# Performance work log

Hardware: AMD Instinct MI355X
Metric: run time of the kernel (lower is better)

Reference implementation:

```python
import jax, jax.numpy as jnp
import numpy as np


def setup_inputs() -> dict:
    key = jax.random.key(0)
    k1, k2, k3 = jax.random.split(key, 3)
    B, C, T = 8, 256, 4096
    H, K = 512, 4
    x = jax.random.normal(k1, (B, C, T), dtype=jnp.float32)
    W = jax.random.normal(k2, (H, C * K), dtype=jnp.float32) * 0.02
    b = jax.random.normal(k3, (H,), dtype=jnp.float32) * 0.02
    return {"x": x, "W": W, "b": b}


def reference(x, W, b):
    # Causal conv1d equivalent of the per-step Linear loop (stride=1).
    # Original flattens window as view(B, C*K): channel-major -> W[h, c*K + k].
    B, C, T = x.shape
    H = W.shape[0]
    K = W.shape[1] // C
    kernel = W.reshape(H, C, K)  # OIH layout
    out = jax.lax.conv_general_dilated(
        x, kernel,
        window_strides=(1,),
        padding=[(K - 1, 0)],  # left-pad only => causal
        dimension_numbers=("NCH", "OIH", "NCH"),
    )
    return out + b[None, :, None]  # (B, H, T)
```

## Files before the change

kernel.cpp:

```cpp
#include <hip/hip_runtime.h>
#include <hip/hip_bf16.h>


#define Bb 8
#define Cc 256
#define Tt 4096
#define Hh 512
#define Kk 4

typedef __attribute__((ext_vector_type(8))) short bf16x8;
typedef __attribute__((ext_vector_type(4))) float f32x4;

#define WS_XT_OFF   0
#define WS_WT_OFF   16777216
#define WS_ZERO_OFF 17825792
#define WS_NEEDED   17826816ULL

__device__ __forceinline__ void gload16(const void* g, void* l) {
    __builtin_amdgcn_global_load_lds(
        (const __attribute__((address_space(1))) void*)g,
        (__attribute__((address_space(3))) void*)l, 16, 0, 0);
}

__global__ __launch_bounds__(256) void prep_kernel(const float* __restrict__ x,
                                                   const float* __restrict__ W,
                                                   __hip_bfloat16* __restrict__ xT,
                                                   __hip_bfloat16* __restrict__ Wt,
                                                   float* __restrict__ zeros) {
    __shared__ __hip_bfloat16 tile[64][72];
    const int bid = blockIdx.x;
    if (bid < 2048) {
        const int t0 = (bid & 63) * 64, c0 = ((bid >> 6) & 3) * 64, b = bid >> 8;
        const int lt = threadIdx.x & 63, lw = threadIdx.x >> 6;
#pragma unroll
        for (int i = 0; i < 16; ++i) {
            int cc = lw + i * 4;
            tile[cc][lt] = __float2bfloat16(x[((size_t)(b * Cc + c0 + cc)) * Tt + t0 + lt]);
        }
        __syncthreads();
#pragma unroll
        for (int i = 0; i < 2; ++i) {
            int tt = (threadIdx.x >> 3) + i * 32;
            int c8 = threadIdx.x & 7;
            short tmp[8];
#pragma unroll
            for (int j = 0; j < 8; ++j) {
                __hip_bfloat16 v = tile[c8 * 8 + j][tt];
                tmp[j] = *reinterpret_cast<short*>(&v);
            }
            *reinterpret_cast<bf16x8*>(&xT[((size_t)(b * Tt + t0 + tt)) * Cc + c0 + c8 * 8]) =
                *reinterpret_cast<bf16x8*>(tmp);
        }
    } else {
        int n = (bid - 2048) * 256 + threadIdx.x;
        int c = n & 255;
        int h = (n >> 8) & 511;
        int k = n >> 17;
        Wt[n] = __float2bfloat16(W[h * (Cc * Kk) + c * Kk + k]);
        if (bid == 2048) zeros[threadIdx.x] = 0.f;
    }
}

#define A_BUF   16384
#define B_BUF   12288
#define B_BASE  49152
#define LDS_TOTAL 73728

#define BAR __builtin_amdgcn_s_barrier()
#define LGKM0 do { asm volatile("s_waitcnt lgkmcnt(0)" ::: "memory"); \
                   __builtin_amdgcn_sched_barrier(0); } while (0)

__global__ __launch_bounds__(256, 2) void conv_mfma_kernel(
    const __hip_bfloat16* __restrict__ xT,
    const __hip_bfloat16* __restrict__ Wt,
    const float* __restrict__ bias,
    const float* __restrict__ zeros,
    float* __restrict__ out)
{
    __shared__ __align__(1024) char smem[LDS_TOTAL];
    const int tid = threadIdx.x, lane = tid & 63, wave = tid >> 6;
    const int wr = wave >> 1, wc = wave & 1;
    const int l15 = lane & 15, lg = lane >> 4;

    const int flat = blockIdx.x + 32 * blockIdx.y + 64 * blockIdx.z;
    const int swz  = (flat & 7) * 64 + (flat >> 3);
    const int t0 = (swz & 31) * 128;
    const int h0 = ((swz >> 5) & 1) * 256;
    const int b  = swz >> 6;

    const char* Wt_c = (const char*)Wt;
    const char* xT_c = (const char*)xT;
    const char* zz   = (const char*)zeros;

    const char* abase[4]; int adst_[4];
#pragma unroll
    for (int i = 0; i < 4; ++i) {
        int s = tid + i * 256;
        int row = s >> 2, sl = s & 3;
        int colch = (sl ^ ((row >> 1) & 3)) * 8;
        abase[i] = Wt_c + (((size_t)(h0 + row)) * Cc + colch) * 2;
        adst_[i] = s * 16;
    }
    const char* bbase[3]; int bdst_[3];
#pragma unroll
    for (int i = 0; i < 3; ++i) {
        int s = tid + i * 256;
        int row = s >> 2, sl = s & 3;
        int colch = (sl ^ ((row >> 1) & 3)) * 8;
        int tg = t0 - 3 + row;
        bool valid = (row <= 130) && (tg >= 0);
        bbase[i] = valid ? xT_c + (((size_t)b * Tt + tg) * Cc + colch) * 2
                         : zz + (s & 31) * 16;
        bdst_[i] = s * 16;
    }

    const int aoff0 = (wr * 128 + l15) * 64 + ((lg ^ ((l15 >> 1) & 3)) << 4);
    int btab[4];
#pragma unroll
    for (int k = 0; k < 4; ++k)
        btab[k] = (wc * 64 + l15 + k) * 64 + ((lg ^ (((l15 + k) >> 1) & 3)) << 4);

    char *A0 = smem, *A1 = smem + A_BUF, *A2 = smem + 2 * A_BUF;
    char *B0 = smem + B_BASE, *B1 = smem + B_BASE + B_BUF;

#pragma unroll
    for (int i = 0; i < 4; ++i) gload16(abase[i], A0 + adst_[i]);
#pragma unroll
    for (int i = 0; i < 3; ++i) gload16(bbase[i], B0 + bdst_[i]);
#pragma unroll
    for (int i = 0; i < 4; ++i) gload16(abase[i] + 262144, A1 + adst_[i]);
    asm volatile("s_waitcnt vmcnt(4)" ::: "memory");
    BAR;

    f32x4 acc[8][4] = {};

#pragma unroll 4
    for (int s = 0; s < 32; ++s) {
        const int kap = s & 3;
        const int bo  = (kap == 0) ? btab[0] : (kap == 1) ? btab[1]
                      : (kap == 2) ? btab[2] : btab[3];

        bf16x8 a_[4], b_[4];
#pragma unroll
        for (int fm = 0; fm < 4; ++fm) a_[fm] = *(const bf16x8*)(A0 + aoff0 + fm * 1024);
#pragma unroll
        for (int ft = 0; ft < 4; ++ft) b_[ft] = *(const bf16x8*)(B0 + bo + ft * 1024);
        if (s < 30) {
            const long au = (long)((s + 2) & 3) * 262144 + (long)((s + 2) >> 2) * 64;
#pragma unroll
            for (int i = 0; i < 4; ++i) gload16(abase[i] + au, A2 + adst_[i]);
        }
        BAR; LGKM0;
        __builtin_amdgcn_s_setprio(1);
#pragma unroll
        for (int fm = 0; fm < 4; ++fm)
#pragma unroll
            for (int ft = 0; ft < 4; ++ft)
                acc[fm][ft] = __builtin_amdgcn_mfma_f32_16x16x32_bf16(a_[fm], b_[ft], acc[fm][ft], 0, 0, 0);
        __builtin_amdgcn_s_setprio(0);
        BAR;
#pragma unroll
        for (int fm = 0; fm < 4; ++fm) a_[fm] = *(const bf16x8*)(A0 + aoff0 + (fm + 4) * 1024);
        if (kap == 0 && s < 28) {
            const long bu = (long)((s >> 2) + 1) * 64;
#pragma unroll
            for (int i = 0; i < 3; ++i) gload16(bbase[i] + bu, B1 + bdst_[i]);
        }
        BAR; LGKM0;
        __builtin_amdgcn_s_setprio(1);
#pragma unroll
        for (int fm = 0; fm < 4; ++fm)
#pragma unroll
            for (int ft = 0; ft < 4; ++ft)
                acc[fm + 4][ft] = __builtin_amdgcn_mfma_f32_16x16x32_bf16(a_[fm], b_[ft], acc[fm + 4][ft], 0, 0, 0);
        __builtin_amdgcn_s_setprio(0);
        if (s < 30) {
            if (kap == 0 && s < 28) asm volatile("s_waitcnt vmcnt(7)" ::: "memory");
            else                    asm volatile("s_waitcnt vmcnt(4)" ::: "memory");
        } else if (s == 30)         asm volatile("s_waitcnt vmcnt(0)" ::: "memory");
        BAR;
        char* tp = A0; A0 = A1; A1 = A2; A2 = tp;
        if (kap == 3) { char* up = B0; B0 = B1; B1 = up; }
    }

#pragma unroll
    for (int fm = 0; fm < 8; ++fm) {
        int hb = h0 + wr * 128 + fm * 16 + lg * 4;
        float4 bs = *(const float4*)&bias[hb];
        const float* bsp = (const float*)&bs;
#pragma unroll
        for (int q = 0; q < 4; ++q)
#pragma unroll
            for (int ft = 0; ft < 4; ++ft) {
                int t = t0 + wc * 64 + ft * 16 + l15;
                out[((size_t)(b * Hh + hb + q)) * Tt + t] = acc[fm][ft][q] + bsp[q];
            }
    }
}

#define TT 256
#define HT 8
#define CT 4
__global__ __launch_bounds__(256) void conv1d_f32_kernel(
    const float* __restrict__ x, const float* __restrict__ W,
    const float* __restrict__ bias, float* __restrict__ out)
{
    const int tid = threadIdx.x;
    const int t0 = blockIdx.x * TT;
    const int h0 = blockIdx.y * HT;
    const int b  = blockIdx.z;
    __shared__ float xs[CT][TT + Kk];
    float acc[HT];
#pragma unroll
    for (int h = 0; h < HT; ++h) acc[h] = 0.f;
    const float* xb = x + (size_t)b * Cc * Tt;
    for (int c0 = 0; c0 < Cc; c0 += CT) {
        __syncthreads();
#pragma unroll
        for (int cc = 0; cc < CT; ++cc)
            for (int j = tid; j < TT + Kk - 1; j += 256) {
                int idx = t0 - (Kk - 1) + j;
                xs[cc][j] = (idx >= 0) ? xb[(size_t)(c0 + cc) * Tt + idx] : 0.f;
            }
        __syncthreads();
#pragma unroll
        for (int cc = 0; cc < CT; ++cc) {
            float xv[Kk];
#pragma unroll
            for (int k = 0; k < Kk; ++k) xv[k] = xs[cc][tid + k];
#pragma unroll
            for (int h = 0; h < HT; ++h) {
                const float* wp = W + (size_t)(h0 + h) * (Cc * Kk) + (size_t)(c0 + cc) * Kk;
#pragma unroll
                for (int k = 0; k < Kk; ++k) acc[h] += wp[k] * xv[k];
            }
        }
    }
#pragma unroll
    for (int h = 0; h < HT; ++h)
        out[((size_t)b * Hh + (h0 + h)) * Tt + t0 + tid] = acc[h] + bias[h0 + h];
}

extern "C" void kernel_launch(void* const* d_in, const int* in_sizes, int n_in,
                              void* d_out, int out_size, void* d_ws, size_t ws_size,
                              hipStream_t stream) {
    const float* x    = (const float*)d_in[0];
    const float* W    = (const float*)d_in[1];
    const float* bias = (const float*)d_in[2];
    float* out        = (float*)d_out;

    if (ws_size >= WS_NEEDED) {
        __hip_bfloat16* xT = (__hip_bfloat16*)((char*)d_ws + WS_XT_OFF);
        __hip_bfloat16* Wt = (__hip_bfloat16*)((char*)d_ws + WS_WT_OFF);
        float* zeros       = (float*)((char*)d_ws + WS_ZERO_OFF);

        prep_kernel<<<dim3(4096), dim3(256), 0, stream>>>(x, W, xT, Wt, zeros);
        conv_mfma_kernel<<<dim3(32, 2, 8), dim3(256), 0, stream>>>(xT, Wt, bias, zeros, out);
    } else {
        conv1d_f32_kernel<<<dim3(Tt / TT, Hh / HT, Bb), dim3(256), 0, stream>>>(x, W, bias, out);
    }
}
```

Before: 51.14 us.

## Fuse x transpose and bf16 conversion into the conv MFMA kernel

Removes the separate pass that transposed x into a (B,T,C) bf16 workspace copy. The conv kernel now reads fp32 x directly through registers, converts it to bf16 and writes swizzled tiles into LDS inside its pipeline. Only the small weight-prep kernel stays. This drops a 32MB read and a 16MB write plus a launch. In exchange it uses strided per-thread global loads, extra VGPRs and manual vmcnt accounting inside the main loop.

```diff
diff --git a/kernel.cpp b/kernel.cpp
--- a/kernel.cpp
+++ b/kernel.cpp
@@ -11,10 +11,7 @@
 typedef __attribute__((ext_vector_type(8))) short bf16x8;
 typedef __attribute__((ext_vector_type(4))) float f32x4;
 
-#define WS_XT_OFF   0
-#define WS_WT_OFF   16777216
-#define WS_ZERO_OFF 17825792
-#define WS_NEEDED   17826816ULL
+#define WS_NEEDED 1048576ULL
 
 __device__ __forceinline__ void gload16(const void* g, void* l) {
     __builtin_amdgcn_global_load_lds(
@@ -22,43 +19,13 @@
         (__attribute__((address_space(3))) void*)l, 16, 0, 0);
 }
 
-__global__ __launch_bounds__(256) void prep_kernel(const float* __restrict__ x,
-                                                   const float* __restrict__ W,
-                                                   __hip_bfloat16* __restrict__ xT,
-                                                   __hip_bfloat16* __restrict__ Wt,
-                                                   float* __restrict__ zeros) {
-    __shared__ __hip_bfloat16 tile[64][72];
-    const int bid = blockIdx.x;
-    if (bid < 2048) {
-        const int t0 = (bid & 63) * 64, c0 = ((bid >> 6) & 3) * 64, b = bid >> 8;
-        const int lt = threadIdx.x & 63, lw = threadIdx.x >> 6;
-#pragma unroll
-        for (int i = 0; i < 16; ++i) {
-            int cc = lw + i * 4;
-            tile[cc][lt] = __float2bfloat16(x[((size_t)(b * Cc + c0 + cc)) * Tt + t0 + lt]);
-        }
-        __syncthreads();
-#pragma unroll
-        for (int i = 0; i < 2; ++i) {
-            int tt = (threadIdx.x >> 3) + i * 32;
-            int c8 = threadIdx.x & 7;
-            short tmp[8];
-#pragma unroll
-            for (int j = 0; j < 8; ++j) {
-                __hip_bfloat16 v = tile[c8 * 8 + j][tt];
-                tmp[j] = *reinterpret_cast<short*>(&v);
-            }
-            *reinterpret_cast<bf16x8*>(&xT[((size_t)(b * Tt + t0 + tt)) * Cc + c0 + c8 * 8]) =
-                *reinterpret_cast<bf16x8*>(tmp);
-        }
-    } else {
-        int n = (bid - 2048) * 256 + threadIdx.x;
-        int c = n & 255;
-        int h = (n >> 8) & 511;
-        int k = n >> 17;
-        Wt[n] = __float2bfloat16(W[h * (Cc * Kk) + c * Kk + k]);
-        if (bid == 2048) zeros[threadIdx.x] = 0.f;
-    }
+__global__ __launch_bounds__(256) void wt_prep_kernel(const float* __restrict__ W,
+                                                      __hip_bfloat16* __restrict__ Wt) {
+    int n = blockIdx.x * 256 + threadIdx.x;
+    int c = n & 255;
+    int h = (n >> 8) & 511;
+    int k = n >> 17;
+    Wt[n] = __float2bfloat16(W[h * (Cc * Kk) + c * Kk + k]);
 }
 
 #define A_BUF   16384
@@ -70,11 +37,44 @@
 #define LGKM0 do { asm volatile("s_waitcnt lgkmcnt(0)" ::: "memory"); \
                    __builtin_amdgcn_sched_barrier(0); } while (0)
 
+#define BLOADS(csb, vv, vvt) do {                                               \
+    int tg_ = t0 - 3 + (tid >> 1);                                              \
+    const float* xp_ = x + ((size_t)(b * Cc + (csb) + (tid & 1) * 16)) * Tt     \
+                         + (tg_ >= 0 ? tg_ : 0);                                \
+    _Pragma("unroll") for (int j = 0; j < 16; ++j) vv[j] = xp_[(size_t)j * Tt]; \
+    if (tg_ < 0) { _Pragma("unroll") for (int j = 0; j < 16; ++j) vv[j] = 0.f; }\
+    if (tid < 6) {                                                              \
+        const float* xq_ = x + ((size_t)(b * Cc + (csb) + (tid & 1) * 16)) * Tt \
+                             + (t0 - 3 + 128 + (tid >> 1));                     \
+        _Pragma("unroll") for (int j = 0; j < 16; ++j) vvt[j] = xq_[(size_t)j * Tt]; \
+    }                                                                           \
+} while (0)
+
+#define BSTORE(dstbuf, vv, vvt) do {                                            \
+    int r_ = tid >> 1, sw_ = (r_ >> 1) & 3, sl0_ = (tid & 1) * 2;               \
+    short o_[16];                                                               \
+    _Pragma("unroll") for (int j = 0; j < 16; ++j) {                            \
+        __hip_bfloat16 h_ = __float2bfloat16(vv[j]);                            \
+        o_[j] = *reinterpret_cast<short*>(&h_);                                 \
+    }                                                                           \
+    *(bf16x8*)((dstbuf) + r_ * 64 + (((sl0_    ) ^ sw_) << 4)) = *(bf16x8*)&o_[0]; \
+    *(bf16x8*)((dstbuf) + r_ * 64 + (((sl0_ + 1) ^ sw_) << 4)) = *(bf16x8*)&o_[8]; \
+    if (tid < 6) {                                                              \
+        int r2_ = 128 + (tid >> 1), sw2_ = (r2_ >> 1) & 3;                      \
+        short p_[16];                                                           \
+        _Pragma("unroll") for (int j = 0; j < 16; ++j) {                        \
+            __hip_bfloat16 h_ = __float2bfloat16(vvt[j]);                       \
+            p_[j] = *reinterpret_cast<short*>(&h_);                             \
+        }                                                                       \
+        *(bf16x8*)((dstbuf) + r2_ * 64 + (((sl0_    ) ^ sw2_) << 4)) = *(bf16x8*)&p_[0]; \
+        *(bf16x8*)((dstbuf) + r2_ * 64 + (((sl0_ + 1) ^ sw2_) << 4)) = *(bf16x8*)&p_[8]; \
+    }                                                                           \
+} while (0)
+
 __global__ __launch_bounds__(256, 2) void conv_mfma_kernel(
-    const __hip_bfloat16* __restrict__ xT,
+    const float* __restrict__ x,
     const __hip_bfloat16* __restrict__ Wt,
     const float* __restrict__ bias,
-    const float* __restrict__ zeros,
     float* __restrict__ out)
 {
     __shared__ __align__(1024) char smem[LDS_TOTAL];
@@ -89,8 +89,6 @@
     const int b  = swz >> 6;
 
     const char* Wt_c = (const char*)Wt;
-    const char* xT_c = (const char*)xT;
-    const char* zz   = (const char*)zeros;
 
     const char* abase[4]; int adst_[4];
 #pragma unroll
@@ -101,18 +99,6 @@
         abase[i] = Wt_c + (((size_t)(h0 + row)) * Cc + colch) * 2;
         adst_[i] = s * 16;
     }
-    const char* bbase[3]; int bdst_[3];
-#pragma unroll
-    for (int i = 0; i < 3; ++i) {
-        int s = tid + i * 256;
-        int row = s >> 2, sl = s & 3;
-        int colch = (sl ^ ((row >> 1) & 3)) * 8;
-        int tg = t0 - 3 + row;
-        bool valid = (row <= 130) && (tg >= 0);
-        bbase[i] = valid ? xT_c + (((size_t)b * Tt + tg) * Cc + colch) * 2
-                         : zz + (s & 31) * 16;
-        bdst_[i] = s * 16;
-    }
 
     const int aoff0 = (wr * 128 + l15) * 64 + ((lg ^ ((l15 >> 1) & 3)) << 4);
     int btab[4];
@@ -123,14 +109,19 @@
     char *A0 = smem, *A1 = smem + A_BUF, *A2 = smem + 2 * A_BUF;
     char *B0 = smem + B_BASE, *B1 = smem + B_BASE + B_BUF;
 
-#pragma unroll
-    for (int i = 0; i < 4; ++i) gload16(abase[i], A0 + adst_[i]);
-#pragma unroll
-    for (int i = 0; i < 3; ++i) gload16(bbase[i], B0 + bdst_[i]);
-#pragma unroll
-    for (int i = 0; i < 4; ++i) gload16(abase[i] + 262144, A1 + adst_[i]);
-    asm volatile("s_waitcnt vmcnt(4)" ::: "memory");
-    BAR;
+    {
+        float pv[16], pvt[16];
+        BLOADS(0, pv, pvt);
+#pragma unroll
+        for (int i = 0; i < 4; ++i) gload16(abase[i], A0 + adst_[i]);
+#pragma unroll
+        for (int i = 0; i < 4; ++i) gload16(abase[i] + 262144, A1 + adst_[i]);
+        asm volatile("s_waitcnt vmcnt(8)" ::: "memory");
+        BSTORE(B0, pv, pvt);
+        asm volatile("s_waitcnt vmcnt(4)" ::: "memory");
+        asm volatile("s_waitcnt lgkmcnt(0)" ::: "memory");
+        BAR;
+    }
 
     f32x4 acc[8][4] = {};
 
@@ -139,12 +130,15 @@
         const int kap = s & 3;
         const int bo  = (kap == 0) ? btab[0] : (kap == 1) ? btab[1]
                       : (kap == 2) ? btab[2] : btab[3];
-
-        bf16x8 a_[4], b_[4];
+        const bool doB = (kap == 0) && (s < 28);
+
+        float bv_[16], bvt_[16];
+        bf16x8 a_[4], bfr_[4];
 #pragma unroll
         for (int fm = 0; fm < 4; ++fm) a_[fm] = *(const bf16x8*)(A0 + aoff0 + fm * 1024);
 #pragma unroll
-        for (int ft = 0; ft < 4; ++ft) b_[ft] = *(const bf16x8*)(B0 + bo + ft * 1024);
+        for (int ft = 0; ft < 4; ++ft) bfr_[ft] = *(const bf16x8*)(B0 + bo + ft * 1024);
+        if (doB) BLOADS(((s >> 2) + 1) * 32, bv_, bvt_);
         if (s < 30) {
             const long au = (long)((s + 2) & 3) * 262144 + (long)((s + 2) >> 2) * 64;
 #pragma unroll
@@ -156,15 +150,14 @@
         for (int fm = 0; fm < 4; ++fm)
 #pragma unroll
             for (int ft = 0; ft < 4; ++ft)
-                acc[fm][ft] = __builtin_amdgcn_mfma_f32_16x16x32_bf16(a_[fm], b_[ft], acc[fm][ft], 0, 0, 0);
+                acc[fm][ft] = __builtin_amdgcn_mfma_f32_16x16x32_bf16(a_[fm], bfr_[ft], acc[fm][ft], 0, 0, 0);
         __builtin_amdgcn_s_setprio(0);
         BAR;
 #pragma unroll
         for (int fm = 0; fm < 4; ++fm) a_[fm] = *(const bf16x8*)(A0 + aoff0 + (fm + 4) * 1024);
-        if (kap == 0 && s < 28) {
-            const long bu = (long)((s >> 2) + 1) * 64;
-#pragma unroll
-            for (int i = 0; i < 3; ++i) gload16(bbase[i] + bu, B1 + bdst_[i]);
+        if (doB) {
+            asm volatile("s_waitcnt vmcnt(4)" ::: "memory");
+            BSTORE(B1, bv_, bvt_);
         }
         BAR; LGKM0;
         __builtin_amdgcn_s_setprio(1);
@@ -172,12 +165,10 @@
         for (int fm = 0; fm < 4; ++fm)
 #pragma unroll
             for (int ft = 0; ft < 4; ++ft)
-                acc[fm + 4][ft] = __builtin_amdgcn_mfma_f32_16x16x32_bf16(a_[fm], b_[ft], acc[fm + 4][ft], 0, 0, 0);
+                acc[fm + 4][ft] = __builtin_amdgcn_mfma_f32_16x16x32_bf16(a_[fm], bfr_[ft], acc[fm + 4][ft], 0, 0, 0);
         __builtin_amdgcn_s_setprio(0);
-        if (s < 30) {
-            if (kap == 0 && s < 28) asm volatile("s_waitcnt vmcnt(7)" ::: "memory");
-            else                    asm volatile("s_waitcnt vmcnt(4)" ::: "memory");
-        } else if (s == 30)         asm volatile("s_waitcnt vmcnt(0)" ::: "memory");
+        if (s < 30)       asm volatile("s_waitcnt vmcnt(4)" ::: "memory");
+        else if (s == 30) asm volatile("s_waitcnt vmcnt(0)" ::: "memory");
         BAR;
         char* tp = A0; A0 = A1; A1 = A2; A2 = tp;
         if (kap == 3) { char* up = B0; B0 = B1; B1 = up; }
@@ -250,12 +241,9 @@
     float* out        = (float*)d_out;
 
     if (ws_size >= WS_NEEDED) {
-        __hip_bfloat16* xT = (__hip_bfloat16*)((char*)d_ws + WS_XT_OFF);
-        __hip_bfloat16* Wt = (__hip_bfloat16*)((char*)d_ws + WS_WT_OFF);
-        float* zeros       = (float*)((char*)d_ws + WS_ZERO_OFF);
-
-        prep_kernel<<<dim3(4096), dim3(256), 0, stream>>>(x, W, xT, Wt, zeros);
-        conv_mfma_kernel<<<dim3(32, 2, 8), dim3(256), 0, stream>>>(xT, Wt, bias, zeros, out);
+        __hip_bfloat16* Wt = (__hip_bfloat16*)d_ws;
+        wt_prep_kernel<<<dim3((Kk * Hh * Cc) / 256), dim3(256), 0, stream>>>(W, Wt);
+        conv_mfma_kernel<<<dim3(32, 2, 8), dim3(256), 0, stream>>>(x, Wt, bias, out);
     } else {
         conv1d_f32_kernel<<<dim3(Tt / TT, Hh / HT, Bb), dim3(256), 0, stream>>>(x, W, bias, out);
     }
```

New measurement: 72.11 us. +41.0%, slower.

## Shrink conv MFMA tile to 128x128 with double-buffered A/B and 3 blocks/CU

Applied to the files above, without the earlier changes.

Halves the per-block H tile from 256 to 128 rows, so there are 1024 blocks instead of 512, and cuts LDS from 72KB to 50KB to allow three blocks per CU. The A pipeline moves from triple to double buffering. Each stage now loads two kernel taps (k pairs), giving 16 iterations instead of 32, with fewer barriers per iteration. The intent is better occupancy and load balance across CUs. The cost is that the x tile is reloaded twice as often, and prefetch depth is shallower, with stricter vmcnt waits.

```diff
diff --git a/kernel.cpp b/kernel.cpp
--- a/kernel.cpp
+++ b/kernel.cpp
@@ -61,16 +61,16 @@
     }
 }
 
-#define A_BUF   16384
-#define B_BUF   12288
-#define B_BASE  49152
-#define LDS_TOTAL 73728
+#define A_BUF    16384
+#define B_BUF    9216
+#define B_BASE   32768
+#define LDS_TOTAL 51200
 
 #define BAR __builtin_amdgcn_s_barrier()
 #define LGKM0 do { asm volatile("s_waitcnt lgkmcnt(0)" ::: "memory"); \
                    __builtin_amdgcn_sched_barrier(0); } while (0)
 
-__global__ __launch_bounds__(256, 2) void conv_mfma_kernel(
+__global__ __launch_bounds__(256, 3) void conv_mfma_kernel(
     const __hip_bfloat16* __restrict__ xT,
     const __hip_bfloat16* __restrict__ Wt,
     const float* __restrict__ bias,
@@ -82,75 +82,81 @@
     const int wr = wave >> 1, wc = wave & 1;
     const int l15 = lane & 15, lg = lane >> 4;
 
-    const int flat = blockIdx.x + 32 * blockIdx.y + 64 * blockIdx.z;
-    const int swz  = (flat & 7) * 64 + (flat >> 3);
-    const int t0 = (swz & 31) * 128;
-    const int h0 = ((swz >> 5) & 1) * 256;
-    const int b  = swz >> 6;
+    const int flat = blockIdx.x + 32 * blockIdx.y + 128 * blockIdx.z;
+    const int nf   = (flat & 7) * 128 + (flat >> 3);
+    const int h0 = (nf & 3) * 128;
+    const int t0 = ((nf >> 2) & 31) * 128;
+    const int b  = nf >> 7;
 
     const char* Wt_c = (const char*)Wt;
     const char* xT_c = (const char*)xT;
     const char* zz   = (const char*)zeros;
 
-    const char* abase[4]; int adst_[4];
+    const char* asrc[4]; int adst_[4];
 #pragma unroll
     for (int i = 0; i < 4; ++i) {
         int s = tid + i * 256;
-        int row = s >> 2, sl = s & 3;
+        int kk = s >> 9, row = (s >> 2) & 127, sl = s & 3;
         int colch = (sl ^ ((row >> 1) & 3)) * 8;
-        abase[i] = Wt_c + (((size_t)(h0 + row)) * Cc + colch) * 2;
+        asrc[i] = Wt_c + (((size_t)(kk * Hh + h0 + row)) * Cc + colch) * 2;
         adst_[i] = s * 16;
     }
-    const char* bbase[3]; int bdst_[3];
+    const char* bsrc[3]; int bdst_[3]; int bstep[3];
 #pragma unroll
     for (int i = 0; i < 3; ++i) {
-        int s = tid + i * 256;
+        int s = (i < 2) ? tid + i * 256 : 512 + lane;
         int row = s >> 2, sl = s & 3;
         int colch = (sl ^ ((row >> 1) & 3)) * 8;
         int tg = t0 - 3 + row;
         bool valid = (row <= 130) && (tg >= 0);
-        bbase[i] = valid ? xT_c + (((size_t)b * Tt + tg) * Cc + colch) * 2
-                         : zz + (s & 31) * 16;
+        bsrc[i]  = valid ? xT_c + (((size_t)b * Tt + tg) * Cc + colch) * 2
+                         : zz + (s & 15) * 16;
+        bstep[i] = valid ? 64 : 0;
         bdst_[i] = s * 16;
     }
 
-    const int aoff0 = (wr * 128 + l15) * 64 + ((lg ^ ((l15 >> 1) & 3)) << 4);
+    const int aoffb = (wr * 64 + l15) * 64 + ((lg ^ ((l15 >> 1) & 3)) << 4);
     int btab[4];
 #pragma unroll
     for (int k = 0; k < 4; ++k)
         btab[k] = (wc * 64 + l15 + k) * 64 + ((lg ^ (((l15 + k) >> 1) & 3)) << 4);
 
-    char *A0 = smem, *A1 = smem + A_BUF, *A2 = smem + 2 * A_BUF;
-    char *B0 = smem + B_BASE, *B1 = smem + B_BASE + B_BUF;
-
-#pragma unroll
-    for (int i = 0; i < 4; ++i) gload16(abase[i], A0 + adst_[i]);
-#pragma unroll
-    for (int i = 0; i < 3; ++i) gload16(bbase[i], B0 + bdst_[i]);
-#pragma unroll
-    for (int i = 0; i < 4; ++i) gload16(abase[i] + 262144, A1 + adst_[i]);
-    asm volatile("s_waitcnt vmcnt(4)" ::: "memory");
+    f32x4 acc[4][4] = {};
+
+#pragma unroll
+    for (int i = 0; i < 4; ++i) gload16(asrc[i], smem + adst_[i]);
+#pragma unroll
+    for (int i = 0; i < 2; ++i) gload16(bsrc[i], smem + B_BASE + bdst_[i]);
+    if (wave == 0) gload16(bsrc[2], smem + B_BASE + bdst_[2]);
+    asm volatile("s_waitcnt vmcnt(0)" ::: "memory");
     BAR;
 
-    f32x4 acc[8][4] = {};
-
-#pragma unroll 4
-    for (int s = 0; s < 32; ++s) {
-        const int kap = s & 3;
-        const int bo  = (kap == 0) ? btab[0] : (kap == 1) ? btab[1]
-                      : (kap == 2) ? btab[2] : btab[3];
+#pragma unroll
+    for (int s = 0; s < 16; ++s) {
+        const int p  = s >> 1;
+        const int kb = 2 * (s & 1);
+        const char* Ab = smem + (s & 1) * A_BUF;
+        const char* Bbf = smem + B_BASE + (p & 1) * B_BUF;
+
+        if (s < 15) {
+            const long aadv = (long)((s + 1) & 1) * 524288 + (long)((s + 1) >> 1) * 64;
+            char* An = smem + ((s + 1) & 1) * A_BUF;
+#pragma unroll
+            for (int i = 0; i < 4; ++i) gload16(asrc[i] + aadv, An + adst_[i]);
+        }
+        if (((s & 1) == 0) && (p < 7)) {
+            char* Bn = smem + B_BASE + ((p + 1) & 1) * B_BUF;
+#pragma unroll
+            for (int i = 0; i < 2; ++i) gload16(bsrc[i] + (p + 1) * bstep[i], Bn + bdst_[i]);
+            if (wave == 0) gload16(bsrc[2] + (p + 1) * bstep[2], Bn + bdst_[2]);
+        }
 
         bf16x8 a_[4], b_[4];
 #pragma unroll
-        for (int fm = 0; fm < 4; ++fm) a_[fm] = *(const bf16x8*)(A0 + aoff0 + fm * 1024);
-#pragma unroll
-        for (int ft = 0; ft < 4; ++ft) b_[ft] = *(const bf16x8*)(B0 + bo + ft * 1024);
-        if (s < 30) {
-            const long au = (long)((s + 2) & 3) * 262144 + (long)((s + 2) >> 2) * 64;
-#pragma unroll
-            for (int i = 0; i < 4; ++i) gload16(abase[i] + au, A2 + adst_[i]);
-        }
-        BAR; LGKM0;
+        for (int fm = 0; fm < 4; ++fm) a_[fm] = *(const bf16x8*)(Ab + aoffb + fm * 1024);
+#pragma unroll
+        for (int ft = 0; ft < 4; ++ft) b_[ft] = *(const bf16x8*)(Bbf + btab[kb] + ft * 1024);
+        LGKM0;
         __builtin_amdgcn_s_setprio(1);
 #pragma unroll
         for (int fm = 0; fm < 4; ++fm)
@@ -158,34 +164,29 @@
             for (int ft = 0; ft < 4; ++ft)
                 acc[fm][ft] = __builtin_amdgcn_mfma_f32_16x16x32_bf16(a_[fm], b_[ft], acc[fm][ft], 0, 0, 0);
         __builtin_amdgcn_s_setprio(0);
-        BAR;
-#pragma unroll
-        for (int fm = 0; fm < 4; ++fm) a_[fm] = *(const bf16x8*)(A0 + aoff0 + (fm + 4) * 1024);
-        if (kap == 0 && s < 28) {
-            const long bu = (long)((s >> 2) + 1) * 64;
-#pragma unroll
-            for (int i = 0; i < 3; ++i) gload16(bbase[i] + bu, B1 + bdst_[i]);
-        }
-        BAR; LGKM0;
+#pragma unroll
+        for (int fm = 0; fm < 4; ++fm) a_[fm] = *(const bf16x8*)(Ab + 8192 + aoffb + fm * 1024);
+#pragma unroll
+        for (int ft = 0; ft < 4; ++ft) b_[ft] = *(const bf16x8*)(Bbf + btab[kb + 1] + ft * 1024);
+        LGKM0;
         __builtin_amdgcn_s_setprio(1);
 #pragma unroll
         for (int fm = 0; fm < 4; ++fm)
 #pragma unroll
             for (int ft = 0; ft < 4; ++ft)
-                acc[fm + 4][ft] = __builtin_amdgcn_mfma_f32_16x16x32_bf16(a_[fm], b_[ft], acc[fm + 4][ft], 0, 0, 0);
+                acc[fm][ft] = __builtin_amdgcn_mfma_f32_16x16x32_bf16(a_[fm], b_[ft], acc[fm][ft], 0, 0, 0);
         __builtin_amdgcn_s_setprio(0);
-        if (s < 30) {
-            if (kap == 0 && s < 28) asm volatile("s_waitcnt vmcnt(7)" ::: "memory");
-            else                    asm volatile("s_waitcnt vmcnt(4)" ::: "memory");
-        } else if (s == 30)         asm volatile("s_waitcnt vmcnt(0)" ::: "memory");
-        BAR;
-        char* tp = A0; A0 = A1; A1 = A2; A2 = tp;
-        if (kap == 3) { char* up = B0; B0 = B1; B1 = up; }
-    }
-
-#pragma unroll
-    for (int fm = 0; fm < 8; ++fm) {
-        int hb = h0 + wr * 128 + fm * 16 + lg * 4;
+
+        if (s < 15) {
+            if (((s & 1) == 0) && (p < 7)) asm volatile("s_waitcnt vmcnt(3)" ::: "memory");
+            else                           asm volatile("s_waitcnt vmcnt(0)" ::: "memory");
+            BAR;
+        }
+    }
+
+#pragma unroll
+    for (int fm = 0; fm < 4; ++fm) {
+        int hb = h0 + wr * 64 + fm * 16 + lg * 4;
         float4 bs = *(const float4*)&bias[hb];
         const float* bsp = (const float*)&bs;
 #pragma unroll
@@ -255,7 +256,7 @@
         float* zeros       = (float*)((char*)d_ws + WS_ZERO_OFF);
 
         prep_kernel<<<dim3(4096), dim3(256), 0, stream>>>(x, W, xT, Wt, zeros);
-        conv_mfma_kernel<<<dim3(32, 2, 8), dim3(256), 0, stream>>>(xT, Wt, bias, zeros, out);
+        conv_mfma_kernel<<<dim3(32, 4, 8), dim3(256), 0, stream>>>(xT, Wt, bias, zeros, out);
     } else {
         conv1d_f32_kernel<<<dim3(Tt / TT, Hh / HT, Bb), dim3(256), 0, stream>>>(x, W, bias, out);
     }
```

Result: faster. 49.91 us (-2.4%).
